# Optimization experiments

Measured on AMD Instinct MI355X. Metric: run time of the kernel, lower is better.

Reference implementation:

```python
import jax, jax.numpy as jnp
import numpy as np

B, C, TX, TY = 32, 384, 512, 2048
NL, K = 2, 3
EPS = 1e-5


def _ln(x, g, b):
    # channel-wise LayerNorm over dim 1 of [B, C, T]
    m = jnp.mean(x, axis=1, keepdims=True)
    v = jnp.mean((x - m) ** 2, axis=1, keepdims=True)
    return (x - m) * jax.lax.rsqrt(v + EPS) * g[None, :, None] + b[None, :, None]


def _conv(x, w, b):
    # x: [B, C, T], w: [O, I, K] -> 'SAME' padding == kernel_size // 2 for odd K
    y = jax.lax.conv_general_dilated(x, w, (1,), 'SAME',
                                     dimension_numbers=('NCH', 'OIH', 'NCH'))
    return y + b[None, :, None]


def _variance_predictor(x, mask, lng, lnb, cw, cb, ow, ob):
    # NL x (LayerNorm -> Conv1d -> SiLU -> [dropout=identity in eval]) * mask
    for i in range(NL):
        h = _conv(_ln(x, lng[i], lnb[i]), cw[i], cb[i])
        x = jax.nn.silu(h) * mask
    return _conv(x, ow, ob) * mask  # [B, 1, T]


def setup_inputs() -> dict:
    key = jax.random.key(0)
    it = iter(jax.random.split(key, 16))
    s = 0.02
    d = {}
    d['x'] = jax.random.normal(next(it), (B, C, TX), jnp.float32)
    d['x_mask'] = jnp.ones((B, 1, TX), jnp.float32)
    d['y_mask'] = jnp.ones((B, 1, TY), jnp.float32)
    d['pitch'] = jax.random.normal(next(it), (B, C, TY), jnp.float32)
    d['energy'] = jax.random.normal(next(it), (B, C, TY), jnp.float32)
    d['path'] = jax.random.uniform(next(it), (B, TX, TY), jnp.float32)
    for p in ('dur', 'pit', 'ene'):
        d[p + '_lng'] = jnp.ones((NL, C), jnp.float32)
        d[p + '_lnb'] = jnp.zeros((NL, C), jnp.float32)
        d[p + '_cw'] = jax.random.normal(next(it), (NL, C, C, K), jnp.float32) * s
        d[p + '_cb'] = jnp.zeros((NL, C), jnp.float32)
        d[p + '_ow'] = jax.random.normal(next(it), (1, C, 1), jnp.float32) * s
        d[p + '_ob'] = jnp.zeros((1,), jnp.float32)
    return d


def reference(x, x_mask, y_mask, pitch, energy, path,
              dur_lng, dur_lnb, dur_cw, dur_cb, dur_ow, dur_ob,
              pit_lng, pit_lnb, pit_cw, pit_cb, pit_ow, pit_ob,
              ene_lng, ene_lnb, ene_cw, ene_cb, ene_ow, ene_ob):
    dur_pred = _variance_predictor(x, x_mask, dur_lng, dur_lnb, dur_cw, dur_cb, dur_ow, dur_ob)
    # LengthRegulator: bmm against duration path matrix [B, TX, TY]
    xe = jnp.einsum('bct,bty->bcy', x, path)  # [B, C, TY]
    pitch_pred = _variance_predictor(xe, y_mask, pit_lng, pit_lnb, pit_cw, pit_cb, pit_ow, pit_ob)
    energy_pred = _variance_predictor(xe, y_mask, ene_lng, ene_lnb, ene_cw, ene_cb, ene_ow, ene_ob)
    out = xe + pitch + energy
    return (out, dur_pred, pitch_pred, energy_pred)
```

## Files before the change

### kernel.cpp

```cpp
#include <hip/hip_runtime.h>

#define B_ 32
#define C_ 384
#define TX_ 512
#define TY_ 2048
#define EPS_ 1e-5f
#define LAY_ ((size_t)(36 * 1536 * 8))

typedef __attribute__((ext_vector_type(8))) short short8;
typedef __attribute__((ext_vector_type(4))) float f32x4;

#define MFMA(a, b, c) __builtin_amdgcn_mfma_f32_16x16x32_bf16(a, b, c, 0, 0, 0)

#define WAITV(N) do { asm volatile("s_waitcnt vmcnt(" #N ")"); \
                      __builtin_amdgcn_sched_barrier(0); } while (0)
#define WAITLK(N) do { asm volatile("s_waitcnt lgkmcnt(" #N ")"); \
                       __builtin_amdgcn_sched_barrier(0); } while (0)
#define SB() __builtin_amdgcn_sched_barrier(0)

typedef unsigned int u32;
__device__ __forceinline__ void gl_lds16(const void* g, void* l) {
    __builtin_amdgcn_global_load_lds(
        (const __attribute__((address_space(1))) u32*)g,
        (__attribute__((address_space(3))) u32*)l, 16, 0, 0);
}

__device__ inline unsigned short f2bf(float f) {
    union { float f; unsigned int u; } v; v.f = f;
    unsigned int r = v.u + 0x7fffu + ((v.u >> 16) & 1u);
    return (unsigned short)(r >> 16);
}
__device__ inline float bf2f(unsigned short s) {
    union { float f; unsigned int u; } v; v.u = ((unsigned int)s) << 16;
    return v.f;
}

template<bool INBF>
__device__ inline float ldx(const void* p, size_t i) {
    if constexpr (INBF) return bf2f(((const unsigned short*)p)[i]);
    else return ((const float*)p)[i];
}

__global__ __launch_bounds__(256) void pack_w2(const float* cw0, const float* cw1,
                                               const float* cw2, const float* g0,
                                               const float* g1, const float* g2,
                                               unsigned short* wp) {
    int idx = blockIdx.x * 256 + threadIdx.x;
    const int NG = 6 * 36 * 384 * 4;
    if (idx >= NG) return;
    int lg = idx & 3;
    int o = (idx >> 2) % 384;
    int c = ((idx >> 2) / 384) % 36;
    int lay = (idx >> 2) / (384 * 36);
    int k = c / 12, ib = c % 12;
    int pr = lay >> 1, l = lay & 1;
    const float* cw = ((pr == 0) ? cw0 : (pr == 1) ? cw1 : cw2) + (size_t)l * C_ * C_ * 3;
    const float* g  = ((pr == 0) ? g0  : (pr == 1) ? g1  : g2)  + (size_t)l * C_;
    const int i0 = ib * 32 + lg * 8;
    short8 v;
    #pragma unroll
    for (int e = 0; e < 8; e++)
        v[e] = (short)f2bf(cw[((size_t)o * C_ + i0 + e) * 3 + k] * g[i0 + e]);
    *(short8*)&wp[(size_t)idx * 8] = v;
}

__global__ __launch_bounds__(256) void bias_fold(
    const float* cw0, const float* cw1, const float* cw2,
    const float* be0, const float* be1, const float* be2,
    const float* cb0, const float* cb1, const float* cb2,
    float* biasT, float* bc0, float* bc2) {
    int idx = blockIdx.x * 256 + threadIdx.x;
    if (idx >= 6 * 384) return;
    int o = idx % 384, lay = idx / 384;
    int pr = lay >> 1, l = lay & 1;
    const float* cw = ((pr == 0) ? cw0 : (pr == 1) ? cw1 : cw2)
                      + (size_t)l * C_ * C_ * 3 + (size_t)o * C_ * 3;
    const float* be = ((pr == 0) ? be0 : (pr == 1) ? be1 : be2) + (size_t)l * C_;
    const float* cb = ((pr == 0) ? cb0 : (pr == 1) ? cb1 : cb2) + (size_t)l * C_;
    float s0 = 0.f, s1 = 0.f, s2 = 0.f;
    for (int i = 0; i < C_; i++) {
        const float b = be[i];
        s0 += cw[i * 3 + 0] * b; s1 += cw[i * 3 + 1] * b; s2 += cw[i * 3 + 2] * b;
    }
    biasT[idx] = cb[o] + s0 + s1 + s2;
    bc0[idx] = s0; bc2[idx] = s2;
}

__global__ __launch_bounds__(256) void pack_x2(const float* x, unsigned short* xp) {
    int idx = blockIdx.x * 256 + threadIdx.x;
    const int NG = B_ * 16 * 384 * 4;
    if (idx >= NG) return;
    int lg = idx & 3;
    int c = (idx >> 2) % 384;
    int q = ((idx >> 2) / 384) % 16;
    int b = (idx >> 2) / (384 * 16);
    const float* src = x + ((size_t)b * C_ + c) * TX_ + q * 32 + lg * 8;
    short8 v;
    #pragma unroll
    for (int e = 0; e < 8; e++) v[e] = (short)f2bf(src[e]);
    *(short8*)&xp[(size_t)idx * 8] = v;
}

__global__ __launch_bounds__(256) void ln_stats_f32(const float* x, float2* st, int T) {
    __shared__ float r1[4][64], r2[4][64];
    int b = blockIdx.y, t0 = blockIdx.x * 64;
    int tl = threadIdx.x & 63, g = threadIdx.x >> 6;
    int t = t0 + tl;
    const float* p = x + (size_t)b * C_ * T + t;
    float s = 0.f, ss = 0.f;
    for (int c = g; c < C_; c += 4) { float v = p[(size_t)c * T]; s += v; ss += v * v; }
    r1[g][tl] = s; r2[g][tl] = ss;
    __syncthreads();
    if (threadIdx.x < 64) {
        float s1 = r1[0][tl] + r1[1][tl] + r1[2][tl] + r1[3][tl];
        float s2 = r2[0][tl] + r2[1][tl] + r2[2][tl] + r2[3][tl];
        float m = s1 * (1.f / C_);
        float var = s2 * (1.f / C_) - m * m;
        st[(size_t)b * T + t0 + tl] = make_float2(m, rsqrtf(var + EPS_));
    }
}

template<bool INBF>
__global__ __launch_bounds__(512, 2) void fused_vp(
    const void* __restrict__ Xin, const float2* __restrict__ stin,
    const unsigned short* __restrict__ W2lay,
    const float* __restrict__ bT,
    const float* __restrict__ c0v, const float* __restrict__ c2v,
    const float* __restrict__ mask,
    float* __restrict__ pred, const float* __restrict__ ow,
    const float* __restrict__ obias, int T)
{
    __shared__ __align__(16) unsigned short xs[132 * 384];
    __shared__ __align__(16) unsigned short wlds[8][2][1536];
    __shared__ float red[260];
    __shared__ float2 st2[130];

    const int tid = threadIdx.x;
    const int b = blockIdx.y;
    const int t0 = blockIdx.x * 128;
    const int lane = tid & 63;
    const int wave = tid >> 6;
    const int lr = lane & 15, lg = lane >> 4;
    const int wm = wave * 48;

    const unsigned short* gbw = W2lay + (size_t)((wm + lr) * 4 + lg) * 8;
    const unsigned short* gbw2 = gbw + LAY_;
    auto STAGE = [&](const unsigned short* base, int c, int buf) {
        #pragma unroll
        for (int fm = 0; fm < 3; fm++)
            gl_lds16(base + (size_t)c * 12288 + fm * 512, &wlds[wave][buf][fm * 512]);
    };
    STAGE(gbw, 0, 0);
    STAGE(gbw, 1, 1);

    {
        const int tl = tid & 127;
        const int tt = 2 + tl;
        const int t = t0 + tl;
        const float2 mr = stin[(size_t)b * T + t];
        const int cg0 = (tid >> 7) * 12;
        for (int i = 0; i < 12; i++) {
            const int cg = cg0 + i;
            const size_t base = ((size_t)b * C_ + cg * 8) * T + t;
            short8 v8;
            #pragma unroll
            for (int j = 0; j < 8; j++)
                v8[j] = (short)f2bf((ldx<INBF>(Xin, base + (size_t)j * T) - mr.x) * mr.y);
            const int ph = (cg & ~7) | ((cg ^ tt) & 7);
            *(short8*)&xs[tt * 384 + ph * 8] = v8;
        }
        if (tid < 192) {
            const int q = tid / 48;
            const int tt2 = (q < 2) ? q : 128 + q;
            const int cg = tid % 48;
            const int t2 = t0 - 2 + tt2;
            short8 v8;
            if (t2 >= 0 && t2 < T) {
                const float2 mr2 = stin[(size_t)b * T + t2];
                const size_t base = ((size_t)b * C_ + cg * 8) * T + t2;
                #pragma unroll
                for (int j = 0; j < 8; j++)
                    v8[j] = (short)f2bf((ldx<INBF>(Xin, base + (size_t)j * T) - mr2.x) * mr2.y);
            } else {
                #pragma unroll
                for (int j = 0; j < 8; j++) v8[j] = 0;
            }
            const int ph = (cg & ~7) | ((cg ^ tt2) & 7);
            *(short8*)&xs[tt2 * 384 + ph * 8] = v8;
        }
    }
    __syncthreads();

    f32x4 acc[3][9];
    const f32x4 zero = {0.f, 0.f, 0.f, 0.f};
    #pragma unroll
    for (int fm = 0; fm < 3; fm++)
        #pragma unroll
        for (int fn = 0; fn < 9; fn++) acc[fm][fn] = zero;

    short8 af[3], bfA[9], bfB[9];
    auto LOADBF1 = [&](short8* dst, int c) {
        const int k = c / 12, ib = c - k * 12;
        const int cgi = ib * 4 + lg;
        #pragma unroll
        for (int fn = 0; fn < 8; fn++) {
            const int row = 1 + fn * 16 + lr + k;
            const int ph = (cgi & ~7) | ((cgi ^ row) & 7);
            dst[fn] = *(const short8*)&xs[row * 384 + ph * 8];
        }
        const int rowh = (lr == 1) ? (129 + k) : k;
        const int phh = (cgi & ~7) | ((cgi ^ rowh) & 7);
        dst[8] = *(const short8*)&xs[rowh * 384 + phh * 8];
    };
    auto LOADAF = [&](int c) {
        #pragma unroll
        for (int fm = 0; fm < 3; fm++)
            af[fm] = *(const short8*)&wlds[wave][c & 1][fm * 512 + lane * 8];
    };
    auto FMAS1 = [&](short8* bf) {
        __builtin_amdgcn_s_setprio(1);
        #pragma unroll
        for (int fm = 0; fm < 3; fm++)
            #pragma unroll
            for (int fn = 0; fn < 9; fn++)
                acc[fm][fn] = MFMA(af[fm], bf[fn], acc[fm][fn]);
        __builtin_amdgcn_s_setprio(0);
    };
    auto STAGE1 = [&](int s) {
        if (s + 2 < 36) STAGE(gbw, s + 2, s & 1);
        else            STAGE(gbw2, s - 34, s & 1);
    };

    LOADBF1(bfA, 0);
    for (int c = 0; c < 36; c += 2) {
        WAITV(3);
        LOADAF(c); SB();
        LOADBF1(bfB, c + 1);
        WAITLK(9);
        STAGE1(c); SB();
        FMAS1(bfA);
        WAITV(3);
        LOADAF(c + 1); SB();
        LOADBF1(bfA, (c + 2 < 36) ? c + 2 : 35);
        WAITLK(9);
        STAGE1(c + 1); SB();
        FMAS1(bfB);
    }

    __syncthreads();
    if (tid < 260) red[tid] = 0.f;
    __syncthreads();

    #pragma unroll
    for (int fn = 0; fn < 8; fn++) {
        const int tt_h = 1 + fn * 16 + lr;
        const int t = t0 + fn * 16 + lr;
        const float mk = mask[(size_t)b * T + t];
        float s1 = 0.f, s2 = 0.f;
        #pragma unroll
        for (int fm = 0; fm < 3; fm++) {
            const int o0 = wm + fm * 16 + lg * 4;
            #pragma unroll
            for (int j = 0; j < 4; j++) {
                float h = acc[fm][fn][j] + bT[o0 + j];
                if (t == 0) h -= c0v[o0 + j];
                if (t == T - 1) h -= c2v[o0 + j];
                const float y = h * (1.f / (1.f + __expf(-h))) * mk;
                acc[fm][fn][j] = y;
                s1 += y; s2 += y * y;
            }
        }
        atomicAdd(&red[tt_h * 2], s1);
        atomicAdd(&red[tt_h * 2 + 1], s2);
    }
    {
        const int tt_h = (lr == 1) ? 129 : 0;
        const int t = t0 - 1 + tt_h;
        const bool inr = (lr < 2) && (t >= 0) && (t < T);
        const float mk = inr ? mask[(size_t)b * T + t] : 0.f;
        float s1 = 0.f, s2 = 0.f;
        #pragma unroll
        for (int fm = 0; fm < 3; fm++) {
            const int o0 = wm + fm * 16 + lg * 4;
            #pragma unroll
            for (int j = 0; j < 4; j++) {
                const float h = acc[fm][8][j] + bT[o0 + j];
                const float y = inr ? (h * (1.f / (1.f + __expf(-h))) * mk) : 0.f;
                acc[fm][8][j] = y;
                s1 += y; s2 += y * y;
            }
        }
        if (inr) {
            atomicAdd(&red[tt_h * 2], s1);
            atomicAdd(&red[tt_h * 2 + 1], s2);
        }
    }
    __syncthreads();

    if (tid < 130) {
        const float s1 = red[tid * 2], s2 = red[tid * 2 + 1];
        const float m = s1 * (1.f / C_);
        const float var = s2 * (1.f / C_) - m * m;
        st2[tid] = make_float2(m, rsqrtf(var + EPS_));
    }
    __syncthreads();

    #pragma unroll
    for (int fn = 0; fn < 8; fn++) {
        const int tt_h = 1 + fn * 16 + lr;
        const float2 mr = st2[tt_h];
        #pragma unroll
        for (int fm = 0; fm < 3; fm++) {
            ushort4 pk;
            #pragma unroll
            for (int j = 0; j < 4; j++)
                ((unsigned short*)&pk)[j] = f2bf((acc[fm][fn][j] - mr.x) * mr.y);
            const int cg = ((wm + fm * 16) >> 3) + (lg >> 1);
            const int ph = (cg & ~7) | ((cg ^ tt_h) & 7);
            *(ushort4*)&xs[tt_h * 384 + ph * 8 + (lg & 1) * 4] = pk;
        }
    }
    if (lr < 2) {
        const int tt_h = (lr == 1) ? 129 : 0;
        const float2 mr = st2[tt_h];
        #pragma unroll
        for (int fm = 0; fm < 3; fm++) {
            ushort4 pk;
            #pragma unroll
            for (int j = 0; j < 4; j++)
                ((unsigned short*)&pk)[j] = f2bf((acc[fm][8][j] - mr.x) * mr.y);
            const int cg = ((wm + fm * 16) >> 3) + (lg >> 1);
            const int ph = (cg & ~7) | ((cg ^ tt_h) & 7);
            *(ushort4*)&xs[tt_h * 384 + ph * 8 + (lg & 1) * 4] = pk;
        }
    }
    __syncthreads();

    f32x4 acc2[3][8];
    #pragma unroll
    for (int fm = 0; fm < 3; fm++)
        #pragma unroll
        for (int fn = 0; fn < 8; fn++) acc2[fm][fn] = zero;

    auto LOADBF2 = [&](short8* dst, int c) {
        const int k = c / 12, ib = c - k * 12;
        const int cgi = ib * 4 + lg;
        #pragma unroll
        for (int fn = 0; fn < 8; fn++) {
            const int row = fn * 16 + lr + k;
            const int ph = (cgi & ~7) | ((cgi ^ row) & 7);
            dst[fn] = *(const short8*)&xs[row * 384 + ph * 8];
        }
    };
    auto FMAS2 = [&](short8* bf) {
        __builtin_amdgcn_s_setprio(1);
        #pragma unroll
        for (int fm = 0; fm < 3; fm++)
            #pragma unroll
            for (int fn = 0; fn < 8; fn++)
                acc2[fm][fn] = MFMA(af[fm], bf[fn], acc2[fm][fn]);
        __builtin_amdgcn_s_setprio(0);
    };
    auto STAGE2 = [&](int s) {
        STAGE(gbw2, (s + 2 < 36) ? s + 2 : 35, s & 1);
    };

    LOADBF2(bfA, 0);
    for (int c = 0; c < 36; c += 2) {
        WAITV(3);
        LOADAF(c); SB();
        LOADBF2(bfB, c + 1);
        WAITLK(8);
        STAGE2(c); SB();
        FMAS2(bfA);
        WAITV(3);
        LOADAF(c + 1); SB();
        LOADBF2(bfA, (c + 2 < 36) ? c + 2 : 35);
        WAITLK(8);
        STAGE2(c + 1); SB();
        FMAS2(bfB);
    }

    __syncthreads();
    if (tid < 128) red[tid] = 0.f;
    __syncthreads();
    #pragma unroll
    for (int fn = 0; fn < 8; fn++) {
        const int tl = fn * 16 + lr;
        const int t = t0 + tl;
        const float mk = mask[(size_t)b * T + t];
        float s1 = 0.f;
        #pragma unroll
        for (int fm = 0; fm < 3; fm++) {
            const int o0 = wm + fm * 16 + lg * 4;
            #pragma unroll
            for (int j = 0; j < 4; j++) {
                float h = acc2[fm][fn][j] + bT[384 + o0 + j];
                if (t == 0) h -= c0v[384 + o0 + j];
                if (t == T - 1) h -= c2v[384 + o0 + j];
                const float y = h * (1.f / (1.f + __expf(-h))) * mk;
                s1 += y * ow[o0 + j];
            }
        }
        atomicAdd(&red[tl], s1);
    }
    __syncthreads();
    if (tid < 128) {
        const int t = t0 + tid;
        pred[(size_t)b * T + t] = (red[tid] + obias[0]) * mask[(size_t)b * T + t];
    }
}

__global__ __launch_bounds__(512, 2) void bmm_ln(
    const unsigned short* __restrict__ x2, const float* __restrict__ path,
    const float* __restrict__ pitch, const float* __restrict__ energy,
    float* __restrict__ out, unsigned short* __restrict__ xebf,
    float2* __restrict__ stout, int fused)
{
    __shared__ __align__(16) char smem[81920];
    unsigned short* ps = (unsigned short*)smem;
    typedef unsigned short wbuf_t[2][1536];
    wbuf_t* wlds = (wbuf_t*)(smem + 32768);
    float* red = (float*)(smem + 49152);

    const int tid = threadIdx.x;
    const int bid = blockIdx.x;
    const int work = (bid & 7) * 64 + (bid >> 3);
    const int b = work >> 4;
    const int y0 = (work & 15) << 7;
    const int lane = tid & 63;
    const int wave = tid >> 6;
    const int lr = lane & 15, lg = lane >> 4;
    const int wm = wave * 48;

    const unsigned short* gbx = x2 + ((size_t)b * 16 * 1536 + (size_t)((wm + lr) * 4 + lg)) * 8;
    auto STAGEW = [&](int u, int buf) {
        #pragma unroll
        for (int fm = 0; fm < 3; fm++)
            gl_lds16(gbx + (size_t)u * 12288 + fm * 512, &wlds[wave][buf][fm * 512]);
    };
    STAGEW(0, 0);
    STAGEW(1, 1);

    auto STAGEP = [&](int s) {
        const int yy = tid & 127;
        const int tg = tid >> 7;
        const float* pb = path + ((size_t)b * TX_ + s * 128 + tg * 32) * TY_ + y0 + yy;
        #pragma unroll
        for (int g = 0; g < 4; g++) {
            float vv[8];
            #pragma unroll
            for (int j = 0; j < 8; j++) vv[j] = pb[(size_t)(g * 8 + j) * TY_];
            short8 v8;
            #pragma unroll
            for (int j = 0; j < 8; j++) v8[j] = (short)f2bf(vv[j]);
            const int cg = tg * 4 + g;
            const int ph = (cg & ~7) | ((cg ^ yy) & 7);
            *(short8*)&ps[yy * 128 + ph * 8] = v8;
        }
    };

    f32x4 acc[3][8];
    const f32x4 zero = {0.f, 0.f, 0.f, 0.f};
    #pragma unroll
    for (int fm = 0; fm < 3; fm++)
        #pragma unroll
        for (int fn = 0; fn < 8; fn++) acc[fm][fn] = zero;

    short8 af[3], bfA[8], bfB[8];
    auto LOADAF = [&](int u) {
        #pragma unroll
        for (int fm = 0; fm < 3; fm++)
            af[fm] = *(const short8*)&wlds[wave][u & 1][fm * 512 + lane * 8];
    };
    auto LOADBF = [&](short8* dst, int uu) {
        const int cgi = uu * 4 + lg;
        #pragma unroll
        for (int fn = 0; fn < 8; fn++) {
            const int row = fn * 16 + lr;
            const int ph = (cgi & ~7) | ((cgi ^ row) & 7);
            dst[fn] = *(const short8*)&ps[row * 128 + ph * 8];
        }
    };
    auto FMAS = [&](short8* bf) {
        __builtin_amdgcn_s_setprio(1);
        #pragma unroll
        for (int fm = 0; fm < 3; fm++)
            #pragma unroll
            for (int fn = 0; fn < 8; fn++)
                acc[fm][fn] = MFMA(af[fm], bf[fn], acc[fm][fn]);
        __builtin_amdgcn_s_setprio(0);
    };

    for (int s = 0; s < 4; ++s) {
        if (s) __syncthreads();
        STAGEP(s);
        __syncthreads();
        const int u0 = s * 4;
        LOADBF(bfA, 0);
        WAITV(3); LOADAF(u0); SB();
        LOADBF(bfB, 1);
        WAITLK(8); STAGEW((u0 + 2 < 16) ? u0 + 2 : 15, u0 & 1); SB();
        FMAS(bfA);
        WAITV(3); LOADAF(u0 + 1); SB();
        LOADBF(bfA, 2);
        WAITLK(8); STAGEW((u0 + 3 < 16) ? u0 + 3 : 15, (u0 + 1) & 1); SB();
        FMAS(bfB);
        WAITV(3); LOADAF(u0 + 2); SB();
        LOADBF(bfB, 3);
        WAITLK(8); STAGEW((u0 + 4 < 16) ? u0 + 4 : 15, (u0 + 2) & 1); SB();
        FMAS(bfA);
        WAITV(3); LOADAF(u0 + 3); SB();
        WAITLK(0); STAGEW((u0 + 5 < 16) ? u0 + 5 : 15, (u0 + 3) & 1); SB();
        FMAS(bfB);
    }
    WAITV(0);

    __syncthreads();
    if (tid < 256) red[tid] = 0.f;
    __syncthreads();
    #pragma unroll
    for (int fn = 0; fn < 8; fn++) {
        const int yl = fn * 16 + lr;
        float s1 = 0.f, s2 = 0.f;
        #pragma unroll
        for (int fm = 0; fm < 3; fm++)
            #pragma unroll
            for (int j = 0; j < 4; j++) {
                const float v = acc[fm][fn][j];
                s1 += v; s2 += v * v;
            }
        atomicAdd(&red[yl * 2], s1);
        atomicAdd(&red[yl * 2 + 1], s2);
    }

    float* psf = (float*)smem;
    for (int r = 0; r < 4; ++r) {
        __syncthreads();
        if ((wave >> 1) == r) {
            const int cbase = (wave & 1) * 48;
            #pragma unroll
            for (int fn = 0; fn < 8; fn++) {
                const int yl = fn * 16 + lr;
                #pragma unroll
                for (int fm = 0; fm < 3; fm++) {
                    const int cl = cbase + fm * 16 + lg * 4;
                    #pragma unroll
                    for (int j = 0; j < 4; j++)
                        psf[(cl + j) * 128 + yl] = acc[fm][fn][j];
                }
            }
        }
        __syncthreads();
        for (int idx = tid; idx < 96 * 32; idx += 512) {
            const int cl = idx >> 5;
            const int y4 = idx & 31;
            const int c = 96 * r + cl;
            const size_t gi = ((size_t)b * C_ + c) * TY_ + y0 + y4 * 4;
            float4 v = ((float4*)&psf[cl * 128])[y4];
            if (fused) {
                const float4 p = *(const float4*)&pitch[gi];
                const float4 e = *(const float4*)&energy[gi];
                float4 o;
                o.x = v.x + p.x + e.x; o.y = v.y + p.y + e.y;
                o.z = v.z + p.z + e.z; o.w = v.w + p.w + e.w;
                *(float4*)&out[gi] = o;
                ushort4 xb;
                xb.x = f2bf(v.x); xb.y = f2bf(v.y); xb.z = f2bf(v.z); xb.w = f2bf(v.w);
                *(ushort4*)&xebf[gi] = xb;
            } else {
                *(float4*)&out[gi] = v;
            }
        }
    }
    __syncthreads();
    if (tid < 128) {
        const int y = y0 + tid;
        const float s1 = red[tid * 2], s2 = red[tid * 2 + 1];
        const float m = s1 * (1.f / C_);
        const float var = s2 * (1.f / C_) - m * m;
        stout[(size_t)b * TY_ + y] = make_float2(m, rsqrtf(var + EPS_));
    }
}

__global__ __launch_bounds__(256) void add3(float4* o, const float4* p, const float4* e, int n4) {
    for (int i = blockIdx.x * 256 + threadIdx.x; i < n4; i += gridDim.x * 256) {
        float4 a = o[i], x1 = p[i], x2 = e[i];
        a.x += x1.x + x2.x; a.y += x1.y + x2.y;
        a.z += x1.z + x2.z; a.w += x1.w + x2.w;
        o[i] = a;
    }
}

extern "C" void kernel_launch(void* const* d_in, const int* in_sizes, int n_in,
                              void* d_out, int out_size, void* d_ws, size_t ws_size,
                              hipStream_t stream)
{
    const float* x      = (const float*)d_in[0];
    const float* x_mask = (const float*)d_in[1];
    const float* y_mask = (const float*)d_in[2];
    const float* pitch  = (const float*)d_in[3];
    const float* energy = (const float*)d_in[4];
    const float* path   = (const float*)d_in[5];
    const float* prm[3][6];
    for (int p = 0; p < 3; p++)
        for (int q = 0; q < 6; q++)
            prm[p][q] = (const float*)d_in[6 + p * 6 + q];

    float* out         = (float*)d_out;
    float* dur_pred    = out + (size_t)B_ * C_ * TY_;
    float* pitch_pred  = dur_pred + B_ * TX_;
    float* energy_pred = pitch_pred + B_ * TY_;

    const size_t BCTY = (size_t)B_ * C_ * TY_;
    char* w = (char*)d_ws;
    auto alloc = [&](size_t bytes) { char* r = w; w += (bytes + 255) & ~(size_t)255; return r; };

    unsigned short* W2   = (unsigned short*)alloc(6 * LAY_ * 2);
    float* biasT         = (float*)alloc(6 * 384 * 4);
    float* bc0           = (float*)alloc(6 * 384 * 4);
    float* bc2           = (float*)alloc(6 * 384 * 4);
    float2* stA          = (float2*)alloc((size_t)B_ * TY_ * 8);
    unsigned short* x2p  = (unsigned short*)alloc((size_t)B_ * 196608 * 2);
    size_t base_end = (size_t)(w - (char*)d_ws);
    unsigned short* xebf = (unsigned short*)alloc(BCTY * 2);
    size_t xe_end = (size_t)(w - (char*)d_ws);

    const bool haveXe = (xe_end <= ws_size);
    if (base_end > ws_size) return;

    pack_w2<<<dim3((6 * 36 * 384 * 4 + 255) / 256), 256, 0, stream>>>(
        prm[0][2], prm[1][2], prm[2][2], prm[0][0], prm[1][0], prm[2][0], W2);
    bias_fold<<<dim3(9), 256, 0, stream>>>(
        prm[0][2], prm[1][2], prm[2][2], prm[0][1], prm[1][1], prm[2][1],
        prm[0][3], prm[1][3], prm[2][3], biasT, bc0, bc2);
    pack_x2<<<dim3((B_ * 16 * 384 * 4 + 255) / 256), 256, 0, stream>>>(x, x2p);
    ln_stats_f32<<<dim3(TX_ / 64, B_), 256, 0, stream>>>(x, stA, TX_);

    fused_vp<false><<<dim3(TX_ / 128, B_), 512, 0, stream>>>(
        x, stA, W2, biasT, bc0, bc2, x_mask,
        dur_pred, prm[0][4], prm[0][5], TX_);

    bmm_ln<<<dim3(512, 1, 1), 512, 0, stream>>>(
        x2p, path, pitch, energy, out, haveXe ? xebf : nullptr, stA, haveXe ? 1 : 0);

    if (haveXe) {
        fused_vp<true><<<dim3(TY_ / 128, B_), 512, 0, stream>>>(
            xebf, stA, W2 + 2 * LAY_, biasT + 2 * 384, bc0 + 2 * 384, bc2 + 2 * 384,
            y_mask, pitch_pred, prm[1][4], prm[1][5], TY_);
        fused_vp<true><<<dim3(TY_ / 128, B_), 512, 0, stream>>>(
            xebf, stA, W2 + 4 * LAY_, biasT + 4 * 384, bc0 + 4 * 384, bc2 + 4 * 384,
            y_mask, energy_pred, prm[2][4], prm[2][5], TY_);
    } else {
        fused_vp<false><<<dim3(TY_ / 128, B_), 512, 0, stream>>>(
            out, stA, W2 + 2 * LAY_, biasT + 2 * 384, bc0 + 2 * 384, bc2 + 2 * 384,
            y_mask, pitch_pred, prm[1][4], prm[1][5], TY_);
        fused_vp<false><<<dim3(TY_ / 128, B_), 512, 0, stream>>>(
            out, stA, W2 + 4 * LAY_, biasT + 4 * 384, bc0 + 4 * 384, bc2 + 4 * 384,
            y_mask, energy_pred, prm[2][4], prm[2][5], TY_);
        add3<<<dim3(2048), 256, 0, stream>>>((float4*)out, (const float4*)pitch,
                                             (const float4*)energy, B_ * C_ * TY_ / 4);
    }
}
```

Measured before the change: 577.3 us.

## Merge prep kernels and co-schedule duration predictor with BMM kernel

```diff
diff --git a/kernel.cpp b/kernel.cpp
--- a/kernel.cpp
+++ b/kernel.cpp
@@ -41,103 +41,99 @@
     else return ((const float*)p)[i];
 }
 
-__global__ __launch_bounds__(256) void pack_w2(const float* cw0, const float* cw1,
-                                               const float* cw2, const float* g0,
-                                               const float* g1, const float* g2,
-                                               unsigned short* wp) {
-    int idx = blockIdx.x * 256 + threadIdx.x;
-    const int NG = 6 * 36 * 384 * 4;
-    if (idx >= NG) return;
-    int lg = idx & 3;
-    int o = (idx >> 2) % 384;
-    int c = ((idx >> 2) / 384) % 36;
-    int lay = (idx >> 2) / (384 * 36);
-    int k = c / 12, ib = c % 12;
-    int pr = lay >> 1, l = lay & 1;
-    const float* cw = ((pr == 0) ? cw0 : (pr == 1) ? cw1 : cw2) + (size_t)l * C_ * C_ * 3;
-    const float* g  = ((pr == 0) ? g0  : (pr == 1) ? g1  : g2)  + (size_t)l * C_;
-    const int i0 = ib * 32 + lg * 8;
-    short8 v;
-    #pragma unroll
-    for (int e = 0; e < 8; e++)
-        v[e] = (short)f2bf(cw[((size_t)o * C_ + i0 + e) * 3 + k] * g[i0 + e]);
-    *(short8*)&wp[(size_t)idx * 8] = v;
-}
-
-__global__ __launch_bounds__(256) void bias_fold(
+__global__ __launch_bounds__(256) void prep_all(
+    const float* x,
     const float* cw0, const float* cw1, const float* cw2,
+    const float* g0, const float* g1, const float* g2,
     const float* be0, const float* be1, const float* be2,
     const float* cb0, const float* cb1, const float* cb2,
-    float* biasT, float* bc0, float* bc2) {
-    int idx = blockIdx.x * 256 + threadIdx.x;
-    if (idx >= 6 * 384) return;
-    int o = idx % 384, lay = idx / 384;
-    int pr = lay >> 1, l = lay & 1;
-    const float* cw = ((pr == 0) ? cw0 : (pr == 1) ? cw1 : cw2)
-                      + (size_t)l * C_ * C_ * 3 + (size_t)o * C_ * 3;
-    const float* be = ((pr == 0) ? be0 : (pr == 1) ? be1 : be2) + (size_t)l * C_;
-    const float* cb = ((pr == 0) ? cb0 : (pr == 1) ? cb1 : cb2) + (size_t)l * C_;
-    float s0 = 0.f, s1 = 0.f, s2 = 0.f;
-    for (int i = 0; i < C_; i++) {
-        const float b = be[i];
-        s0 += cw[i * 3 + 0] * b; s1 += cw[i * 3 + 1] * b; s2 += cw[i * 3 + 2] * b;
-    }
-    biasT[idx] = cb[o] + s0 + s1 + s2;
-    bc0[idx] = s0; bc2[idx] = s2;
+    unsigned short* wp, unsigned short* xp, float2* stA,
+    float* biasT, float* bc0, float* bc2)
+{
+    __shared__ float r1[4][64], r2[4][64];
+    const int bid = blockIdx.x;
+    const int tid = threadIdx.x;
+
+    if (bid < 1296) {
+        int idx = bid * 256 + tid;
+        const int NG = 6 * 36 * 384 * 4;
+        if (idx >= NG) return;
+        int lg = idx & 3;
+        int o = (idx >> 2) % 384;
+        int c = ((idx >> 2) / 384) % 36;
+        int lay = (idx >> 2) / (384 * 36);
+        int k = c / 12, ib = c % 12;
+        int pr = lay >> 1, l = lay & 1;
+        const float* cw = ((pr == 0) ? cw0 : (pr == 1) ? cw1 : cw2) + (size_t)l * C_ * C_ * 3;
+        const float* g  = ((pr == 0) ? g0  : (pr == 1) ? g1  : g2)  + (size_t)l * C_;
+        const int i0 = ib * 32 + lg * 8;
+        short8 v;
+        #pragma unroll
+        for (int e = 0; e < 8; e++)
+            v[e] = (short)f2bf(cw[((size_t)o * C_ + i0 + e) * 3 + k] * g[i0 + e]);
+        *(short8*)&wp[(size_t)idx * 8] = v;
+    } else if (bid < 4368) {
+        int idx = (bid - 1296) * 256 + tid;
+        const int NG = B_ * 16 * 384 * 4;
+        if (idx >= NG) return;
+        int lg = idx & 3;
+        int c = (idx >> 2) % 384;
+        int q = ((idx >> 2) / 384) % 16;
+        int b = (idx >> 2) / (384 * 16);
+        const float* src = x + ((size_t)b * C_ + c) * TX_ + q * 32 + lg * 8;
+        short8 v;
+        #pragma unroll
+        for (int e = 0; e < 8; e++) v[e] = (short)f2bf(src[e]);
+        *(short8*)&xp[(size_t)idx * 8] = v;
+    } else if (bid < 4624) {
+        const int q = bid - 4368;
+        const int b = q >> 3, t0 = (q & 7) * 64;
+        const int tl = tid & 63, g = tid >> 6;
+        const int t = t0 + tl;
+        const float* p = x + (size_t)b * C_ * TX_ + t;
+        float s = 0.f, ss = 0.f;
+        for (int c = g; c < C_; c += 4) { float v = p[(size_t)c * TX_]; s += v; ss += v * v; }
+        r1[g][tl] = s; r2[g][tl] = ss;
+        __syncthreads();
+        if (tid < 64) {
+            float s1 = r1[0][tl] + r1[1][tl] + r1[2][tl] + r1[3][tl];
+            float s2 = r2[0][tl] + r2[1][tl] + r2[2][tl] + r2[3][tl];
+            float m = s1 * (1.f / C_);
+            float var = s2 * (1.f / C_) - m * m;
+            stA[(size_t)b * TX_ + t0 + tl] = make_float2(m, rsqrtf(var + EPS_));
+        }
+    } else {
+        int idx = (bid - 4624) * 256 + tid;
+        if (idx >= 6 * 384) return;
+        int o = idx % 384, lay = idx / 384;
+        int pr = lay >> 1, l = lay & 1;
+        const float* cw = ((pr == 0) ? cw0 : (pr == 1) ? cw1 : cw2)
+                          + (size_t)l * C_ * C_ * 3 + (size_t)o * C_ * 3;
+        const float* be = ((pr == 0) ? be0 : (pr == 1) ? be1 : be2) + (size_t)l * C_;
+        const float* cb = ((pr == 0) ? cb0 : (pr == 1) ? cb1 : cb2) + (size_t)l * C_;
+        float s0 = 0.f, s1 = 0.f, s2 = 0.f;
+        for (int i = 0; i < C_; i++) {
+            const float b = be[i];
+            s0 += cw[i * 3 + 0] * b; s1 += cw[i * 3 + 1] * b; s2 += cw[i * 3 + 2] * b;
+        }
+        biasT[idx] = cb[o] + s0 + s1 + s2;
+        bc0[idx] = s0; bc2[idx] = s2;
+    }
 }
 
-__global__ __launch_bounds__(256) void pack_x2(const float* x, unsigned short* xp) {
-    int idx = blockIdx.x * 256 + threadIdx.x;
-    const int NG = B_ * 16 * 384 * 4;
-    if (idx >= NG) return;
-    int lg = idx & 3;
-    int c = (idx >> 2) % 384;
-    int q = ((idx >> 2) / 384) % 16;
-    int b = (idx >> 2) / (384 * 16);
-    const float* src = x + ((size_t)b * C_ + c) * TX_ + q * 32 + lg * 8;
-    short8 v;
-    #pragma unroll
-    for (int e = 0; e < 8; e++) v[e] = (short)f2bf(src[e]);
-    *(short8*)&xp[(size_t)idx * 8] = v;
-}
-
-__global__ __launch_bounds__(256) void ln_stats_f32(const float* x, float2* st, int T) {
-    __shared__ float r1[4][64], r2[4][64];
-    int b = blockIdx.y, t0 = blockIdx.x * 64;
-    int tl = threadIdx.x & 63, g = threadIdx.x >> 6;
-    int t = t0 + tl;
-    const float* p = x + (size_t)b * C_ * T + t;
-    float s = 0.f, ss = 0.f;
-    for (int c = g; c < C_; c += 4) { float v = p[(size_t)c * T]; s += v; ss += v * v; }
-    r1[g][tl] = s; r2[g][tl] = ss;
-    __syncthreads();
-    if (threadIdx.x < 64) {
-        float s1 = r1[0][tl] + r1[1][tl] + r1[2][tl] + r1[3][tl];
-        float s2 = r2[0][tl] + r2[1][tl] + r2[2][tl] + r2[3][tl];
-        float m = s1 * (1.f / C_);
-        float var = s2 * (1.f / C_) - m * m;
-        st[(size_t)b * T + t0 + tl] = make_float2(m, rsqrtf(var + EPS_));
-    }
-}
-
 template<bool INBF>
-__global__ __launch_bounds__(512, 2) void fused_vp(
-    const void* __restrict__ Xin, const float2* __restrict__ stin,
-    const unsigned short* __restrict__ W2lay,
-    const float* __restrict__ bT,
-    const float* __restrict__ c0v, const float* __restrict__ c2v,
-    const float* __restrict__ mask,
-    float* __restrict__ pred, const float* __restrict__ ow,
-    const float* __restrict__ obias, int T)
+__device__ void vp64_body(char* smem,
+    const void* Xin, const float2* stin,
+    const unsigned short* W2lay, const float* bT,
+    const float* c0v, const float* c2v, const float* mask,
+    float* pred, const float* ow, const float* obias,
+    int T, int b, int t0)
 {
-    __shared__ __align__(16) unsigned short xs[132 * 384];
-    __shared__ __align__(16) unsigned short wlds[8][2][1536];
-    __shared__ float red[260];
-    __shared__ float2 st2[130];
+    unsigned short* xs = (unsigned short*)smem;
+    float* red = (float*)(smem + 52224);
+    float2* st2 = (float2*)(smem + 52224 + 544);
 
     const int tid = threadIdx.x;
-    const int b = blockIdx.y;
-    const int t0 = blockIdx.x * 128;
     const int lane = tid & 63;
     const int wave = tid >> 6;
     const int lr = lane & 15, lg = lane >> 4;
@@ -145,22 +141,13 @@
 
     const unsigned short* gbw = W2lay + (size_t)((wm + lr) * 4 + lg) * 8;
     const unsigned short* gbw2 = gbw + LAY_;
-    auto STAGE = [&](const unsigned short* base, int c, int buf) {
-        #pragma unroll
-        for (int fm = 0; fm < 3; fm++)
-            gl_lds16(base + (size_t)c * 12288 + fm * 512, &wlds[wave][buf][fm * 512]);
-    };
-    STAGE(gbw, 0, 0);
-    STAGE(gbw, 1, 1);
 
     {
-        const int tl = tid & 127;
-        const int tt = 2 + tl;
-        const int t = t0 + tl;
+        const int tt = 2 + lane;
+        const int t = t0 + lane;
         const float2 mr = stin[(size_t)b * T + t];
-        const int cg0 = (tid >> 7) * 12;
-        for (int i = 0; i < 12; i++) {
-            const int cg = cg0 + i;
+        for (int i = 0; i < 6; i++) {
+            const int cg = wave + 8 * i;
             const size_t base = ((size_t)b * C_ + cg * 8) * T + t;
             short8 v8;
             #pragma unroll
@@ -171,7 +158,7 @@
         }
         if (tid < 192) {
             const int q = tid / 48;
-            const int tt2 = (q < 2) ? q : 128 + q;
+            const int tt2 = (q < 2) ? q : 64 + q;
             const int cg = tid % 48;
             const int t2 = t0 - 2 + tt2;
             short8 v8;
@@ -191,68 +178,57 @@
     }
     __syncthreads();
 
-    f32x4 acc[3][9];
+    f32x4 acc[3][5];
     const f32x4 zero = {0.f, 0.f, 0.f, 0.f};
     #pragma unroll
     for (int fm = 0; fm < 3; fm++)
         #pragma unroll
-        for (int fn = 0; fn < 9; fn++) acc[fm][fn] = zero;
-
-    short8 af[3], bfA[9], bfB[9];
-    auto LOADBF1 = [&](short8* dst, int c) {
+        for (int fn = 0; fn < 5; fn++) acc[fm][fn] = zero;
+
+    short8 afA[3], afB[3], bf[5];
+    auto LOADW = [&](short8* d, const unsigned short* base, int c) {
+        #pragma unroll
+        for (int fm = 0; fm < 3; fm++)
+            d[fm] = *(const short8*)(base + (size_t)c * 12288 + fm * 512);
+    };
+    auto LOADBF1 = [&](int c) {
         const int k = c / 12, ib = c - k * 12;
         const int cgi = ib * 4 + lg;
         #pragma unroll
-        for (int fn = 0; fn < 8; fn++) {
+        for (int fn = 0; fn < 4; fn++) {
             const int row = 1 + fn * 16 + lr + k;
             const int ph = (cgi & ~7) | ((cgi ^ row) & 7);
-            dst[fn] = *(const short8*)&xs[row * 384 + ph * 8];
-        }
-        const int rowh = (lr == 1) ? (129 + k) : k;
+            bf[fn] = *(const short8*)&xs[row * 384 + ph * 8];
+        }
+        const int rowh = (lr == 1) ? (65 + k) : k;
         const int phh = (cgi & ~7) | ((cgi ^ rowh) & 7);
-        dst[8] = *(const short8*)&xs[rowh * 384 + phh * 8];
-    };
-    auto LOADAF = [&](int c) {
-        #pragma unroll
-        for (int fm = 0; fm < 3; fm++)
-            af[fm] = *(const short8*)&wlds[wave][c & 1][fm * 512 + lane * 8];
-    };
-    auto FMAS1 = [&](short8* bf) {
+        bf[4] = *(const short8*)&xs[rowh * 384 + phh * 8];
+    };
+    auto FMAS1 = [&](short8* af) {
         __builtin_amdgcn_s_setprio(1);
         #pragma unroll
         for (int fm = 0; fm < 3; fm++)
             #pragma unroll
-            for (int fn = 0; fn < 9; fn++)
+            for (int fn = 0; fn < 5; fn++)
                 acc[fm][fn] = MFMA(af[fm], bf[fn], acc[fm][fn]);
         __builtin_amdgcn_s_setprio(0);
     };
-    auto STAGE1 = [&](int s) {
-        if (s + 2 < 36) STAGE(gbw, s + 2, s & 1);
-        else            STAGE(gbw2, s - 34, s & 1);
-    };
-
-    LOADBF1(bfA, 0);
-    for (int c = 0; c < 36; c += 2) {
-        WAITV(3);
-        LOADAF(c); SB();
-        LOADBF1(bfB, c + 1);
-        WAITLK(9);
-        STAGE1(c); SB();
-        FMAS1(bfA);
-        WAITV(3);
-        LOADAF(c + 1); SB();
-        LOADBF1(bfA, (c + 2 < 36) ? c + 2 : 35);
-        WAITLK(9);
-        STAGE1(c + 1); SB();
-        FMAS1(bfB);
-    }
-
-    __syncthreads();
-    if (tid < 260) red[tid] = 0.f;
-    __syncthreads();
-
-    #pragma unroll
-    for (int fn = 0; fn < 8; fn++) {
+
+    LOADW(afA, gbw, 0);
+    #pragma unroll 2
+    for (int c = 0; c < 36; ++c) {
+        const unsigned short* nb = (c + 1 < 36) ? gbw : gbw2;
+        const int nc = (c + 1 < 36) ? c + 1 : 0;
+        if ((c & 1) == 0) { LOADW(afB, nb, nc); LOADBF1(c); FMAS1(afA); }
+        else              { LOADW(afA, nb, nc); LOADBF1(c); FMAS1(afB); }
+    }
+
+    __syncthreads();
+    if (tid < 132) red[tid] = 0.f;
+    __syncthreads();
+
+    #pragma unroll
+    for (int fn = 0; fn < 4; fn++) {
         const int tt_h = 1 + fn * 16 + lr;
         const int t = t0 + fn * 16 + lr;
         const float mk = mask[(size_t)b * T + t];
@@ -274,7 +250,7 @@
         atomicAdd(&red[tt_h * 2 + 1], s2);
     }
     {
-        const int tt_h = (lr == 1) ? 129 : 0;
+        const int tt_h = (lr == 1) ? 65 : 0;
         const int t = t0 - 1 + tt_h;
         const bool inr = (lr < 2) && (t >= 0) && (t < T);
         const float mk = inr ? mask[(size_t)b * T + t] : 0.f;
@@ -284,9 +260,9 @@
             const int o0 = wm + fm * 16 + lg * 4;
             #pragma unroll
             for (int j = 0; j < 4; j++) {
-                const float h = acc[fm][8][j] + bT[o0 + j];
+                const float h = acc[fm][4][j] + bT[o0 + j];
                 const float y = inr ? (h * (1.f / (1.f + __expf(-h))) * mk) : 0.f;
-                acc[fm][8][j] = y;
+                acc[fm][4][j] = y;
                 s1 += y; s2 += y * y;
             }
         }
@@ -297,7 +273,7 @@
     }
     __syncthreads();
 
-    if (tid < 130) {
+    if (tid < 66) {
         const float s1 = red[tid * 2], s2 = red[tid * 2 + 1];
         const float m = s1 * (1.f / C_);
         const float var = s2 * (1.f / C_) - m * m;
@@ -306,7 +282,7 @@
     __syncthreads();
 
     #pragma unroll
-    for (int fn = 0; fn < 8; fn++) {
+    for (int fn = 0; fn < 4; fn++) {
         const int tt_h = 1 + fn * 16 + lr;
         const float2 mr = st2[tt_h];
         #pragma unroll
@@ -321,14 +297,14 @@
         }
     }
     if (lr < 2) {
-        const int tt_h = (lr == 1) ? 129 : 0;
+        const int tt_h = (lr == 1) ? 65 : 0;
         const float2 mr = st2[tt_h];
         #pragma unroll
         for (int fm = 0; fm < 3; fm++) {
             ushort4 pk;
             #pragma unroll
             for (int j = 0; j < 4; j++)
-                ((unsigned short*)&pk)[j] = f2bf((acc[fm][8][j] - mr.x) * mr.y);
+                ((unsigned short*)&pk)[j] = f2bf((acc[fm][4][j] - mr.x) * mr.y);
             const int cg = ((wm + fm * 16) >> 3) + (lg >> 1);
             const int ph = (cg & ~7) | ((cg ^ tt_h) & 7);
             *(ushort4*)&xs[tt_h * 384 + ph * 8 + (lg & 1) * 4] = pk;
@@ -336,56 +312,44 @@
     }
     __syncthreads();
 
-    f32x4 acc2[3][8];
+    f32x4 acc2[3][4];
     #pragma unroll
     for (int fm = 0; fm < 3; fm++)
         #pragma unroll
-        for (int fn = 0; fn < 8; fn++) acc2[fm][fn] = zero;
-
-    auto LOADBF2 = [&](short8* dst, int c) {
+        for (int fn = 0; fn < 4; fn++) acc2[fm][fn] = zero;
+
+    auto LOADBF2 = [&](int c) {
         const int k = c / 12, ib = c - k * 12;
         const int cgi = ib * 4 + lg;
         #pragma unroll
-        for (int fn = 0; fn < 8; fn++) {
+        for (int fn = 0; fn < 4; fn++) {
             const int row = fn * 16 + lr + k;
             const int ph = (cgi & ~7) | ((cgi ^ row) & 7);
-            dst[fn] = *(const short8*)&xs[row * 384 + ph * 8];
-        }
-    };
-    auto FMAS2 = [&](short8* bf) {
+            bf[fn] = *(const short8*)&xs[row * 384 + ph * 8];
+        }
+    };
+    auto FMAS2 = [&](short8* af) {
         __builtin_amdgcn_s_setprio(1);
         #pragma unroll
         for (int fm = 0; fm < 3; fm++)
             #pragma unroll
-            for (int fn = 0; fn < 8; fn++)
+            for (int fn = 0; fn < 4; fn++)
                 acc2[fm][fn] = MFMA(af[fm], bf[fn], acc2[fm][fn]);
         __builtin_amdgcn_s_setprio(0);
     };
-    auto STAGE2 = [&](int s) {
-        STAGE(gbw2, (s + 2 < 36) ? s + 2 : 35, s & 1);
-    };
-
-    LOADBF2(bfA, 0);
-    for (int c = 0; c < 36; c += 2) {
-        WAITV(3);
-        LOADAF(c); SB();
-        LOADBF2(bfB, c + 1);
-        WAITLK(8);
-        STAGE2(c); SB();
-        FMAS2(bfA);
-        WAITV(3);
-        LOADAF(c + 1); SB();
-        LOADBF2(bfA, (c + 2 < 36) ? c + 2 : 35);
-        WAITLK(8);
-        STAGE2(c + 1); SB();
-        FMAS2(bfB);
-    }
-
-    __syncthreads();
-    if (tid < 128) red[tid] = 0.f;
-    __syncthreads();
-    #pragma unroll
-    for (int fn = 0; fn < 8; fn++) {
+
+    #pragma unroll 2
+    for (int c = 0; c < 36; ++c) {
+        const int nc = (c + 1 < 36) ? c + 1 : 35;
+        if ((c & 1) == 0) { LOADW(afB, gbw2, nc); LOADBF2(c); FMAS2(afA); }
+        else              { LOADW(afA, gbw2, nc); LOADBF2(c); FMAS2(afB); }
+    }
+
+    __syncthreads();
+    if (tid < 64) red[tid] = 0.f;
+    __syncthreads();
+    #pragma unroll
+    for (int fn = 0; fn < 4; fn++) {
         const int tl = fn * 16 + lr;
         const int t = t0 + tl;
         const float mk = mask[(size_t)b * T + t];
@@ -405,19 +369,32 @@
         atomicAdd(&red[tl], s1);
     }
     __syncthreads();
-    if (tid < 128) {
+    if (tid < 64) {
         const int t = t0 + tid;
         pred[(size_t)b * T + t] = (red[tid] + obias[0]) * mask[(size_t)b * T + t];
     }
 }
 
-__global__ __launch_bounds__(512, 2) void bmm_ln(
+__global__ __launch_bounds__(512, 2) void bmm_vptx(
     const unsigned short* __restrict__ x2, const float* __restrict__ path,
     const float* __restrict__ pitch, const float* __restrict__ energy,
     float* __restrict__ out, unsigned short* __restrict__ xebf,
-    float2* __restrict__ stout, int fused)
+    float2* __restrict__ stB, int fused,
+    const float* __restrict__ xf, const float2* __restrict__ stA,
+    const unsigned short* __restrict__ W2, const float* __restrict__ biasT,
+    const float* __restrict__ bc0, const float* __restrict__ bc2,
+    const float* __restrict__ x_mask, float* __restrict__ dur_pred,
+    const float* __restrict__ dow, const float* __restrict__ dob)
 {
     __shared__ __align__(16) char smem[81920];
+
+    if (blockIdx.x >= 512) {
+        const int v = blockIdx.x - 512;
+        vp64_body<false>(smem, xf, stA, W2, biasT, bc0, bc2, x_mask,
+                         dur_pred, dow, dob, TX_, v >> 3, (v & 7) * 64);
+        return;
+    }
+
     unsigned short* ps = (unsigned short*)smem;
     typedef unsigned short wbuf_t[2][1536];
     wbuf_t* wlds = (wbuf_t*)(smem + 32768);
@@ -579,7 +556,307 @@
         const float s1 = red[tid * 2], s2 = red[tid * 2 + 1];
         const float m = s1 * (1.f / C_);
         const float var = s2 * (1.f / C_) - m * m;
-        stout[(size_t)b * TY_ + y] = make_float2(m, rsqrtf(var + EPS_));
+        stB[(size_t)b * TY_ + y] = make_float2(m, rsqrtf(var + EPS_));
+    }
+}
+
+template<bool INBF>
+__global__ __launch_bounds__(512, 2) void vp128(
+    const void* __restrict__ Xin, const float2* __restrict__ stin,
+    const unsigned short* __restrict__ W2full, const float* __restrict__ biasT,
+    const float* __restrict__ bc0f, const float* __restrict__ bc2f,
+    const float* __restrict__ mask,
+    float* __restrict__ pred1, float* __restrict__ pred2,
+    const float* __restrict__ ow1, const float* __restrict__ ow2,
+    const float* __restrict__ ob1, const float* __restrict__ ob2, int T)
+{
+    __shared__ __align__(16) unsigned short xs[132 * 384];
+    __shared__ __align__(16) unsigned short wlds[8][2][1536];
+    __shared__ float red[260];
+    __shared__ float2 st2[130];
+
+    const int z = blockIdx.z;
+    const unsigned short* W2lay = W2full + (size_t)(2 + 2 * z) * LAY_;
+    const float* bT  = biasT + (2 + 2 * z) * 384;
+    const float* c0v = bc0f  + (2 + 2 * z) * 384;
+    const float* c2v = bc2f  + (2 + 2 * z) * 384;
+    float* pred = z ? pred2 : pred1;
+    const float* ow = z ? ow2 : ow1;
+    const float* obias = z ? ob2 : ob1;
+
+    const int tid = threadIdx.x;
+    const int b = blockIdx.y;
+    const int t0 = blockIdx.x * 128;
+    const int lane = tid & 63;
+    const int wave = tid >> 6;
+    const int lr = lane & 15, lg = lane >> 4;
+    const int wm = wave * 48;
+
+    const unsigned short* gbw = W2lay + (size_t)((wm + lr) * 4 + lg) * 8;
+    const unsigned short* gbw2 = gbw + LAY_;
+    auto STAGE = [&](const unsigned short* base, int c, int buf) {
+        #pragma unroll
+        for (int fm = 0; fm < 3; fm++)
+            gl_lds16(base + (size_t)c * 12288 + fm * 512, &wlds[wave][buf][fm * 512]);
+    };
+    STAGE(gbw, 0, 0);
+    STAGE(gbw, 1, 1);
+
+    {
+        const int tl = tid & 127;
+        const int tt = 2 + tl;
+        const int t = t0 + tl;
+        const float2 mr = stin[(size_t)b * T + t];
+        const int cg0 = (tid >> 7) * 12;
+        for (int i = 0; i < 12; i++) {
+            const int cg = cg0 + i;
+            const size_t base = ((size_t)b * C_ + cg * 8) * T + t;
+            short8 v8;
+            #pragma unroll
+            for (int j = 0; j < 8; j++)
+                v8[j] = (short)f2bf((ldx<INBF>(Xin, base + (size_t)j * T) - mr.x) * mr.y);
+            const int ph = (cg & ~7) | ((cg ^ tt) & 7);
+            *(short8*)&xs[tt * 384 + ph * 8] = v8;
+        }
+        if (tid < 192) {
+            const int q = tid / 48;
+            const int tt2 = (q < 2) ? q : 128 + q;
+            const int cg = tid % 48;
+            const int t2 = t0 - 2 + tt2;
+            short8 v8;
+            if (t2 >= 0 && t2 < T) {
+                const float2 mr2 = stin[(size_t)b * T + t2];
+                const size_t base = ((size_t)b * C_ + cg * 8) * T + t2;
+                #pragma unroll
+                for (int j = 0; j < 8; j++)
+                    v8[j] = (short)f2bf((ldx<INBF>(Xin, base + (size_t)j * T) - mr2.x) * mr2.y);
+            } else {
+                #pragma unroll
+                for (int j = 0; j < 8; j++) v8[j] = 0;
+            }
+            const int ph = (cg & ~7) | ((cg ^ tt2) & 7);
+            *(short8*)&xs[tt2 * 384 + ph * 8] = v8;
+        }
+    }
+    __syncthreads();
+
+    f32x4 acc[3][9];
+    const f32x4 zero = {0.f, 0.f, 0.f, 0.f};
+    #pragma unroll
+    for (int fm = 0; fm < 3; fm++)
+        #pragma unroll
+        for (int fn = 0; fn < 9; fn++) acc[fm][fn] = zero;
+
+    short8 af[3], bfA[9], bfB[9];
+    auto LOADBF1 = [&](short8* dst, int c) {
+        const int k = c / 12, ib = c - k * 12;
+        const int cgi = ib * 4 + lg;
+        #pragma unroll
+        for (int fn = 0; fn < 8; fn++) {
+            const int row = 1 + fn * 16 + lr + k;
+            const int ph = (cgi & ~7) | ((cgi ^ row) & 7);
+            dst[fn] = *(const short8*)&xs[row * 384 + ph * 8];
+        }
+        const int rowh = (lr == 1) ? (129 + k) : k;
+        const int phh = (cgi & ~7) | ((cgi ^ rowh) & 7);
+        dst[8] = *(const short8*)&xs[rowh * 384 + phh * 8];
+    };
+    auto LOADAF = [&](int c) {
+        #pragma unroll
+        for (int fm = 0; fm < 3; fm++)
+            af[fm] = *(const short8*)&wlds[wave][c & 1][fm * 512 + lane * 8];
+    };
+    auto FMAS1 = [&](short8* bf) {
+        __builtin_amdgcn_s_setprio(1);
+        #pragma unroll
+        for (int fm = 0; fm < 3; fm++)
+            #pragma unroll
+            for (int fn = 0; fn < 9; fn++)
+                acc[fm][fn] = MFMA(af[fm], bf[fn], acc[fm][fn]);
+        __builtin_amdgcn_s_setprio(0);
+    };
+    auto STAGE1 = [&](int s) {
+        if (s + 2 < 36) STAGE(gbw, s + 2, s & 1);
+        else            STAGE(gbw2, s - 34, s & 1);
+    };
+
+    LOADBF1(bfA, 0);
+    for (int c = 0; c < 36; c += 2) {
+        WAITV(3);
+        LOADAF(c); SB();
+        LOADBF1(bfB, c + 1);
+        WAITLK(9);
+        STAGE1(c); SB();
+        FMAS1(bfA);
+        WAITV(3);
+        LOADAF(c + 1); SB();
+        LOADBF1(bfA, (c + 2 < 36) ? c + 2 : 35);
+        WAITLK(9);
+        STAGE1(c + 1); SB();
+        FMAS1(bfB);
+    }
+
+    __syncthreads();
+    if (tid < 260) red[tid] = 0.f;
+    __syncthreads();
+
+    #pragma unroll
+    for (int fn = 0; fn < 8; fn++) {
+        const int tt_h = 1 + fn * 16 + lr;
+        const int t = t0 + fn * 16 + lr;
+        const float mk = mask[(size_t)b * T + t];
+        float s1 = 0.f, s2 = 0.f;
+        #pragma unroll
+        for (int fm = 0; fm < 3; fm++) {
+            const int o0 = wm + fm * 16 + lg * 4;
+            #pragma unroll
+            for (int j = 0; j < 4; j++) {
+                float h = acc[fm][fn][j] + bT[o0 + j];
+                if (t == 0) h -= c0v[o0 + j];
+                if (t == T - 1) h -= c2v[o0 + j];
+                const float y = h * (1.f / (1.f + __expf(-h))) * mk;
+                acc[fm][fn][j] = y;
+                s1 += y; s2 += y * y;
+            }
+        }
+        atomicAdd(&red[tt_h * 2], s1);
+        atomicAdd(&red[tt_h * 2 + 1], s2);
+    }
+    {
+        const int tt_h = (lr == 1) ? 129 : 0;
+        const int t = t0 - 1 + tt_h;
+        const bool inr = (lr < 2) && (t >= 0) && (t < T);
+        const float mk = inr ? mask[(size_t)b * T + t] : 0.f;
+        float s1 = 0.f, s2 = 0.f;
+        #pragma unroll
+        for (int fm = 0; fm < 3; fm++) {
+            const int o0 = wm + fm * 16 + lg * 4;
+            #pragma unroll
+            for (int j = 0; j < 4; j++) {
+                const float h = acc[fm][8][j] + bT[o0 + j];
+                const float y = inr ? (h * (1.f / (1.f + __expf(-h))) * mk) : 0.f;
+                acc[fm][8][j] = y;
+                s1 += y; s2 += y * y;
+            }
+        }
+        if (inr) {
+            atomicAdd(&red[tt_h * 2], s1);
+            atomicAdd(&red[tt_h * 2 + 1], s2);
+        }
+    }
+    __syncthreads();
+
+    if (tid < 130) {
+        const float s1 = red[tid * 2], s2 = red[tid * 2 + 1];
+        const float m = s1 * (1.f / C_);
+        const float var = s2 * (1.f / C_) - m * m;
+        st2[tid] = make_float2(m, rsqrtf(var + EPS_));
+    }
+    __syncthreads();
+
+    #pragma unroll
+    for (int fn = 0; fn < 8; fn++) {
+        const int tt_h = 1 + fn * 16 + lr;
+        const float2 mr = st2[tt_h];
+        #pragma unroll
+        for (int fm = 0; fm < 3; fm++) {
+            ushort4 pk;
+            #pragma unroll
+            for (int j = 0; j < 4; j++)
+                ((unsigned short*)&pk)[j] = f2bf((acc[fm][fn][j] - mr.x) * mr.y);
+            const int cg = ((wm + fm * 16) >> 3) + (lg >> 1);
+            const int ph = (cg & ~7) | ((cg ^ tt_h) & 7);
+            *(ushort4*)&xs[tt_h * 384 + ph * 8 + (lg & 1) * 4] = pk;
+        }
+    }
+    if (lr < 2) {
+        const int tt_h = (lr == 1) ? 129 : 0;
+        const float2 mr = st2[tt_h];
+        #pragma unroll
+        for (int fm = 0; fm < 3; fm++) {
+            ushort4 pk;
+            #pragma unroll
+            for (int j = 0; j < 4; j++)
+                ((unsigned short*)&pk)[j] = f2bf((acc[fm][8][j] - mr.x) * mr.y);
+            const int cg = ((wm + fm * 16) >> 3) + (lg >> 1);
+            const int ph = (cg & ~7) | ((cg ^ tt_h) & 7);
+            *(ushort4*)&xs[tt_h * 384 + ph * 8 + (lg & 1) * 4] = pk;
+        }
+    }
+    __syncthreads();
+
+    f32x4 acc2[3][8];
+    #pragma unroll
+    for (int fm = 0; fm < 3; fm++)
+        #pragma unroll
+        for (int fn = 0; fn < 8; fn++) acc2[fm][fn] = zero;
+
+    auto LOADBF2 = [&](short8* dst, int c) {
+        const int k = c / 12, ib = c - k * 12;
+        const int cgi = ib * 4 + lg;
+        #pragma unroll
+        for (int fn = 0; fn < 8; fn++) {
+            const int row = fn * 16 + lr + k;
+            const int ph = (cgi & ~7) | ((cgi ^ row) & 7);
+            dst[fn] = *(const short8*)&xs[row * 384 + ph * 8];
+        }
+    };
+    auto FMAS2 = [&](short8* bf) {
+        __builtin_amdgcn_s_setprio(1);
+        #pragma unroll
+        for (int fm = 0; fm < 3; fm++)
+            #pragma unroll
+            for (int fn = 0; fn < 8; fn++)
+                acc2[fm][fn] = MFMA(af[fm], bf[fn], acc2[fm][fn]);
+        __builtin_amdgcn_s_setprio(0);
+    };
+    auto STAGE2 = [&](int s) {
+        STAGE(gbw2, (s + 2 < 36) ? s + 2 : 35, s & 1);
+    };
+
+    LOADBF2(bfA, 0);
+    for (int c = 0; c < 36; c += 2) {
+        WAITV(3);
+        LOADAF(c); SB();
+        LOADBF2(bfB, c + 1);
+        WAITLK(8);
+        STAGE2(c); SB();
+        FMAS2(bfA);
+        WAITV(3);
+        LOADAF(c + 1); SB();
+        LOADBF2(bfA, (c + 2 < 36) ? c + 2 : 35);
+        WAITLK(8);
+        STAGE2(c + 1); SB();
+        FMAS2(bfB);
+    }
+
+    __syncthreads();
+    if (tid < 128) red[tid] = 0.f;
+    __syncthreads();
+    #pragma unroll
+    for (int fn = 0; fn < 8; fn++) {
+        const int tl = fn * 16 + lr;
+        const int t = t0 + tl;
+        const float mk = mask[(size_t)b * T + t];
+        float s1 = 0.f;
+        #pragma unroll
+        for (int fm = 0; fm < 3; fm++) {
+            const int o0 = wm + fm * 16 + lg * 4;
+            #pragma unroll
+            for (int j = 0; j < 4; j++) {
+                float h = acc2[fm][fn][j] + bT[384 + o0 + j];
+                if (t == 0) h -= c0v[384 + o0 + j];
+                if (t == T - 1) h -= c2v[384 + o0 + j];
+                const float y = h * (1.f / (1.f + __expf(-h))) * mk;
+                s1 += y * ow[o0 + j];
+            }
+        }
+        atomicAdd(&red[tl], s1);
+    }
+    __syncthreads();
+    if (tid < 128) {
+        const int t = t0 + tid;
+        pred[(size_t)b * T + t] = (red[tid] + obias[0]) * mask[(size_t)b * T + t];
     }
 }
 
@@ -621,6 +898,7 @@
     float* bc0           = (float*)alloc(6 * 384 * 4);
     float* bc2           = (float*)alloc(6 * 384 * 4);
     float2* stA          = (float2*)alloc((size_t)B_ * TY_ * 8);
+    float2* stB          = (float2*)alloc((size_t)B_ * TY_ * 8);
     unsigned short* x2p  = (unsigned short*)alloc((size_t)B_ * 196608 * 2);
     size_t base_end = (size_t)(w - (char*)d_ws);
     unsigned short* xebf = (unsigned short*)alloc(BCTY * 2);
@@ -629,35 +907,24 @@
     const bool haveXe = (xe_end <= ws_size);
     if (base_end > ws_size) return;
 
-    pack_w2<<<dim3((6 * 36 * 384 * 4 + 255) / 256), 256, 0, stream>>>(
-        prm[0][2], prm[1][2], prm[2][2], prm[0][0], prm[1][0], prm[2][0], W2);
-    bias_fold<<<dim3(9), 256, 0, stream>>>(
-        prm[0][2], prm[1][2], prm[2][2], prm[0][1], prm[1][1], prm[2][1],
-        prm[0][3], prm[1][3], prm[2][3], biasT, bc0, bc2);
-    pack_x2<<<dim3((B_ * 16 * 384 * 4 + 255) / 256), 256, 0, stream>>>(x, x2p);
-    ln_stats_f32<<<dim3(TX_ / 64, B_), 256, 0, stream>>>(x, stA, TX_);
-
-    fused_vp<false><<<dim3(TX_ / 128, B_), 512, 0, stream>>>(
-        x, stA, W2, biasT, bc0, bc2, x_mask,
-        dur_pred, prm[0][4], prm[0][5], TX_);
-
-    bmm_ln<<<dim3(512, 1, 1), 512, 0, stream>>>(
-        x2p, path, pitch, energy, out, haveXe ? xebf : nullptr, stA, haveXe ? 1 : 0);
+    prep_all<<<dim3(4633), 256, 0, stream>>>(
+        x, prm[0][2], prm[1][2], prm[2][2], prm[0][0], prm[1][0], prm[2][0],
+        prm[0][1], prm[1][1], prm[2][1], prm[0][3], prm[1][3], prm[2][3],
+        W2, x2p, stA, biasT, bc0, bc2);
+
+    bmm_vptx<<<dim3(768), 512, 0, stream>>>(
+        x2p, path, pitch, energy, out, haveXe ? xebf : nullptr, stB,
+        haveXe ? 1 : 0, x, stA, W2, biasT, bc0, bc2, x_mask,
+        dur_pred, prm[0][4], prm[0][5]);
 
     if (haveXe) {
-        fused_vp<true><<<dim3(TY_ / 128, B_), 512, 0, stream>>>(
-            xebf, stA, W2 + 2 * LAY_, biasT + 2 * 384, bc0 + 2 * 384, bc2 + 2 * 384,
-            y_mask, pitch_pred, prm[1][4], prm[1][5], TY_);
-        fused_vp<true><<<dim3(TY_ / 128, B_), 512, 0, stream>>>(
-            xebf, stA, W2 + 4 * LAY_, biasT + 4 * 384, bc0 + 4 * 384, bc2 + 4 * 384,
-            y_mask, energy_pred, prm[2][4], prm[2][5], TY_);
+        vp128<true><<<dim3(TY_ / 128, B_, 2), 512, 0, stream>>>(
+            xebf, stB, W2, biasT, bc0, bc2, y_mask,
+            pitch_pred, energy_pred, prm[1][4], prm[2][4], prm[1][5], prm[2][5], TY_);
     } else {
-        fused_vp<false><<<dim3(TY_ / 128, B_), 512, 0, stream>>>(
-            out, stA, W2 + 2 * LAY_, biasT + 2 * 384, bc0 + 2 * 384, bc2 + 2 * 384,
-            y_mask, pitch_pred, prm[1][4], prm[1][5], TY_);
-        fused_vp<false><<<dim3(TY_ / 128, B_), 512, 0, stream>>>(
-            out, stA, W2 + 4 * LAY_, biasT + 4 * 384, bc0 + 4 * 384, bc2 + 4 * 384,
-            y_mask, energy_pred, prm[2][4], prm[2][5], TY_);
+        vp128<false><<<dim3(TY_ / 128, B_, 2), 512, 0, stream>>>(
+            out, stB, W2, biasT, bc0, bc2, y_mask,
+            pitch_pred, energy_pred, prm[1][4], prm[2][4], prm[1][5], prm[2][5], TY_);
         add3<<<dim3(2048), 256, 0, stream>>>((float4*)out, (const float4*)pitch,
                                              (const float4*)energy, B_ * C_ * TY_ / 4);
     }
```

New measurement: 524.4 us. 1.1x faster.
